# Performance work log

Hardware: AMD Instinct MI355X
Metric: run time of the kernel (lower is better)

The kernel has to match this reference:

```python
import jax, jax.numpy as jnp
import numpy as np

W_LOSS = 10.0
THRESHOLD = 1.0
ACOS_EPS = 1e-7


def _normalize(v, eps=1e-8):
    n = jnp.linalg.norm(v, axis=-1, keepdims=True)
    return v / jnp.maximum(n, eps)


def quat_to_rotmat(q):
    # q: (..., 4) in (w, x, y, z) order, as in Zhou et al. / EPN repo
    q = _normalize(q)
    w, x, y, z = q[..., 0], q[..., 1], q[..., 2], q[..., 3]
    R = jnp.stack([
        1 - 2 * (y * y + z * z), 2 * (x * y - z * w), 2 * (x * z + y * w),
        2 * (x * y + z * w), 1 - 2 * (x * x + z * z), 2 * (y * z - x * w),
        2 * (x * z - y * w), 2 * (y * z + x * w), 1 - 2 * (x * x + y * y),
    ], axis=-1)
    return R.reshape(q.shape[:-1] + (3, 3))


def acos_safe(x):
    return jnp.arccos(jnp.clip(x, -1.0 + ACOS_EPS, 1.0 - ACOS_EPS))


def angle_from_R(R):
    # R: (..., 3, 3) -> geodesic angle via trace
    tr = jnp.trace(R, axis1=-2, axis2=-1)
    return acos_safe(0.5 * (tr - 1.0))


def setup_inputs() -> dict:
    key = jax.random.key(0)
    k1, k2, k3, k4, k5 = jax.random.split(key, 5)
    B, NA, NR = 32768, 60, 4
    wts = jax.random.normal(k1, (B, NA), dtype=jnp.float32)
    label = jax.random.randint(k2, (B,), 0, NA, dtype=jnp.int64)
    y = jax.random.normal(k3, (B, NR, NA), dtype=jnp.float32)
    # gt_R and anchors are valid rotation matrices (via random quaternions)
    gt_R = quat_to_rotmat(jax.random.normal(k4, (B, NA, 4), dtype=jnp.float32))
    anchors = quat_to_rotmat(jax.random.normal(k5, (NA, 4), dtype=jnp.float32))
    return {"wts": wts, "label": label, "y": y, "gt_R": gt_R, "anchors": anchors}


def reference(wts, label, y, gt_R, anchors):
    b, na = wts.shape
    nr = y.shape[1]
    true_R = gt_R[:, 29]  # (b, 3, 3)

    # --- CrossEntropyLoss branch (classifier) ---
    logp = jax.nn.log_softmax(wts, axis=1)
    cls_loss = -jnp.mean(jnp.take_along_axis(logp, label[:, None], axis=1))
    preds = jnp.argmax(wts, axis=1)  # (b,)
    r_acc = jnp.mean((preds == label).astype(jnp.float32))

    # --- anchor-wise predicted rotations ---
    # y (b, nr, na) -> (b, na, nr) -> (b, na, 3, 3)
    pred_RAnchor = quat_to_rotmat(jnp.swapaxes(y, 1, 2))

    gt_bias = angle_from_R(gt_R)  # (b, na)
    mask = (gt_bias < THRESHOLD).astype(gt_R.dtype)[:, :, None, None]
    l2_loss = jnp.sum(jnp.square(gt_R * mask - pred_RAnchor * mask))
    loss = cls_loss + W_LOSS * l2_loss

    # --- final predicted rotation: gather best anchor, compose with anchor rot ---
    sel = jnp.take_along_axis(pred_RAnchor, preds[:, None, None, None], axis=1)[:, 0]  # (b,3,3)
    pred_R = jnp.einsum('bij,bjk->bik', anchors[preds], sel)

    # --- mean angular error ---
    ang_err = angle_from_R(jnp.einsum('bij,bkj->bik', pred_R, true_R))  # (b,)

    return (loss, cls_loss, W_LOSS * l2_loss, r_acc, ang_err)
```

## Files before the change

kernel.cpp:

```cpp
#include <hip/hip_runtime.h>
#include <math.h>

constexpr int Bc  = 32768;
constexpr int NAc = 60;
constexpr int NRc = 4;

constexpr int WPB    = 4;
constexpr int NBLK   = 2048;
constexpr int NWAVES = NBLK * WPB;

#define COS_ONE 0.5403023058681398f

__global__ __launch_bounds__(256) void mtl_main(
    const float* __restrict__ wts,
    const int*   __restrict__ label,
    const float* __restrict__ y,
    const float* __restrict__ gt_R,
    const float* __restrict__ anchors,
    float*       __restrict__ out,
    float*       __restrict__ l2p,
    float*       __restrict__ lpp,
    float*       __restrict__ crp)
{
    const int lane = threadIdx.x & 63;
    const int wave = threadIdx.x >> 6;
    const int gw   = blockIdx.x * WPB + wave;

    float l2_acc = 0.0f;
    float lp_acc = 0.0f;
    float cr_acc = 0.0f;

    for (int b = gw; b < Bc; b += NWAVES) {
        float w = -INFINITY;
        if (lane < NAc) w = wts[(size_t)b * NAc + lane];
        float mv = w;
        int   mi = lane;
        for (int off = 32; off; off >>= 1) {
            float ov = __shfl_xor(mv, off, 64);
            int   oi = __shfl_xor(mi, off, 64);
            if (ov > mv || (ov == mv && oi < mi)) { mv = ov; mi = oi; }
        }
        float e  = (lane < NAc) ? expf(w - mv) : 0.0f;
        float se = e;
        for (int off = 32; off; off >>= 1) se += __shfl_xor(se, off, 64);
        float lse  = mv + logf(se);
        int   lab  = label[b];
        float wlab = __shfl(w, lab, 64);
        if (lane == 0) {
            lp_acc += wlab - lse;
            cr_acc += (mi == lab) ? 1.0f : 0.0f;
        }

        if (lane < NAc) {
            const float* yb = y + (size_t)b * (NRc * NAc);
            float qw = yb[0 * NAc + lane];
            float qx = yb[1 * NAc + lane];
            float qy = yb[2 * NAc + lane];
            float qz = yb[3 * NAc + lane];
            float n   = sqrtf(qw * qw + qx * qx + qy * qy + qz * qz);
            float inv = 1.0f / fmaxf(n, 1e-8f);
            qw *= inv; qx *= inv; qy *= inv; qz *= inv;

            float R00 = 1.0f - 2.0f * (qy * qy + qz * qz);
            float R01 = 2.0f * (qx * qy - qz * qw);
            float R02 = 2.0f * (qx * qz + qy * qw);
            float R10 = 2.0f * (qx * qy + qz * qw);
            float R11 = 1.0f - 2.0f * (qx * qx + qz * qz);
            float R12 = 2.0f * (qy * qz - qx * qw);
            float R20 = 2.0f * (qx * qz - qy * qw);
            float R21 = 2.0f * (qy * qz + qx * qw);
            float R22 = 1.0f - 2.0f * (qx * qx + qy * qy);

            const float* g = gt_R + ((size_t)b * NAc + lane) * 9;
            float g0 = g[0], g1 = g[1], g2 = g[2];
            float g3 = g[3], g4 = g[4], g5 = g[5];
            float g6 = g[6], g7 = g[7], g8 = g[8];

            float xb = 0.5f * (g0 + g4 + g8 - 1.0f);
            if (xb > COS_ONE) {
                float d0 = g0 - R00, d1 = g1 - R01, d2 = g2 - R02;
                float d3 = g3 - R10, d4 = g4 - R11, d5 = g5 - R12;
                float d6 = g6 - R20, d7 = g7 - R21, d8 = g8 - R22;
                l2_acc += d0 * d0 + d1 * d1 + d2 * d2
                        + d3 * d3 + d4 * d4 + d5 * d5
                        + d6 * d6 + d7 * d7 + d8 * d8;
            }

            if (lane == mi) {
                const float* A = anchors + (size_t)mi * 9;
                float a0 = A[0], a1 = A[1], a2 = A[2];
                float a3 = A[3], a4 = A[4], a5 = A[5];
                float a6 = A[6], a7 = A[7], a8 = A[8];
                float P00 = a0 * R00 + a1 * R10 + a2 * R20;
                float P01 = a0 * R01 + a1 * R11 + a2 * R21;
                float P02 = a0 * R02 + a1 * R12 + a2 * R22;
                float P10 = a3 * R00 + a4 * R10 + a5 * R20;
                float P11 = a3 * R01 + a4 * R11 + a5 * R21;
                float P12 = a3 * R02 + a4 * R12 + a5 * R22;
                float P20 = a6 * R00 + a7 * R10 + a8 * R20;
                float P21 = a6 * R01 + a7 * R11 + a8 * R21;
                float P22 = a6 * R02 + a7 * R12 + a8 * R22;
                const float* tR = gt_R + ((size_t)b * NAc + 29) * 9;
                float tr = P00 * tR[0] + P01 * tR[1] + P02 * tR[2]
                         + P10 * tR[3] + P11 * tR[4] + P12 * tR[5]
                         + P20 * tR[6] + P21 * tR[7] + P22 * tR[8];
                float cx = 0.5f * (tr - 1.0f);
                cx = fminf(fmaxf(cx, -1.0f + 1e-7f), 1.0f - 1e-7f);
                out[4 + b] = acosf(cx);
            }
        }
    }

    for (int off = 32; off; off >>= 1) {
        l2_acc += __shfl_xor(l2_acc, off, 64);
        lp_acc += __shfl_xor(lp_acc, off, 64);
        cr_acc += __shfl_xor(cr_acc, off, 64);
    }
    __shared__ float s_l2[WPB], s_lp[WPB], s_cr[WPB];
    if (lane == 0) { s_l2[wave] = l2_acc; s_lp[wave] = lp_acc; s_cr[wave] = cr_acc; }
    __syncthreads();
    if (threadIdx.x == 0) {
        float t2 = 0.0f, tp = 0.0f, tc = 0.0f;
        for (int i = 0; i < WPB; ++i) { t2 += s_l2[i]; tp += s_lp[i]; tc += s_cr[i]; }
        l2p[blockIdx.x] = t2;
        lpp[blockIdx.x] = tp;
        crp[blockIdx.x] = tc;
    }
}

__global__ __launch_bounds__(64) void mtl_final(
    const float* __restrict__ l2p,
    const float* __restrict__ lpp,
    const float* __restrict__ crp,
    float*       __restrict__ out)
{
    const int lane = threadIdx.x;
    double l2 = 0.0, lp = 0.0, cr = 0.0;
    for (int i = lane; i < NBLK; i += 64) {
        l2 += (double)l2p[i];
        lp += (double)lpp[i];
        cr += (double)crp[i];
    }
    for (int off = 32; off; off >>= 1) {
        l2 += __shfl_xor(l2, off, 64);
        lp += __shfl_xor(lp, off, 64);
        cr += __shfl_xor(cr, off, 64);
    }
    if (lane == 0) {
        float cls = (float)(-lp / (double)Bc);
        float l2s = (float)(10.0 * l2);
        out[0] = cls + l2s;
        out[1] = cls;
        out[2] = l2s;
        out[3] = (float)(cr / (double)Bc);
    }
}

extern "C" void kernel_launch(void* const* d_in, const int* in_sizes, int n_in,
                              void* d_out, int out_size, void* d_ws, size_t ws_size,
                              hipStream_t stream) {
    const float* wts     = (const float*)d_in[0];
    const int*   label   = (const int*)d_in[1];
    const float* y       = (const float*)d_in[2];
    const float* gt_R    = (const float*)d_in[3];
    const float* anchors = (const float*)d_in[4];
    float* out = (float*)d_out;

    float* l2p = (float*)d_ws;
    float* lpp = l2p + NBLK;
    float* crp = lpp + NBLK;

    mtl_main<<<NBLK, 256, 0, stream>>>(wts, label, y, gt_R, anchors, out, l2p, lpp, crp);
    mtl_final<<<1, 64, 0, stream>>>(l2p, lpp, crp, out);
}
```

Baseline: 156.5 us.

## Split L2 loss into flat tiled kernel with LDS-staged coalesced gt_R loads

Splits the fused per-sample kernel in two. A flat per-(sample, anchor) L2 kernel stages 256 gt_R matrices into shared memory with float4 coalesced loads. A separate classifier and angle-error kernel computes the rotation only for the argmax lane. This removes the stride-9 uncoalesced gt_R reads and the idle lanes (60 of 64) in the heavy pass, at the cost of an extra kernel launch and re-reading y for the selected anchor.

```diff
diff --git a/kernel.cpp b/kernel.cpp
--- a/kernel.cpp
+++ b/kernel.cpp
@@ -5,32 +5,98 @@
 constexpr int NAc = 60;
 constexpr int NRc = 4;
 
-constexpr int WPB    = 4;
-constexpr int NBLK   = 2048;
-constexpr int NWAVES = NBLK * WPB;
+constexpr int NP     = Bc * NAc;
+constexpr int TILE   = 256;
+constexpr int NTILES = NP / TILE;
+constexpr int K1_BLOCKS = 3840;
+constexpr int K2_BLOCKS = 1024;
+constexpr int K2_WAVES  = K2_BLOCKS * 4;
 
 #define COS_ONE 0.5403023058681398f
 
-__global__ __launch_bounds__(256) void mtl_main(
+__global__ __launch_bounds__(256) void l2_pairs(
+    const float* __restrict__ y,
+    const float* __restrict__ gt_R,
+    float*       __restrict__ l2p)
+{
+    __shared__ float4 sg4[TILE * 9 / 4];
+    float* sg = (float*)sg4;
+    const int tid = threadIdx.x;
+
+    float acc = 0.0f;
+
+    for (int tile = blockIdx.x; tile < NTILES; tile += gridDim.x) {
+        __syncthreads();
+        const float4* gbase = (const float4*)(gt_R + (size_t)tile * (TILE * 9));
+        for (int i = tid; i < TILE * 9 / 4; i += 256) sg4[i] = gbase[i];
+        __syncthreads();
+
+        const int p = tile * TILE + tid;
+        const int b = p / NAc;
+        const int a = p - b * NAc;
+
+        const float* yb = y + (size_t)b * (NRc * NAc) + a;
+        float qw = yb[0 * NAc];
+        float qx = yb[1 * NAc];
+        float qy = yb[2 * NAc];
+        float qz = yb[3 * NAc];
+
+        const float* g = sg + tid * 9;
+        float g0 = g[0], g1 = g[1], g2 = g[2];
+        float g3 = g[3], g4 = g[4], g5 = g[5];
+        float g6 = g[6], g7 = g[7], g8 = g[8];
+
+        float n   = sqrtf(qw * qw + qx * qx + qy * qy + qz * qz);
+        float inv = 1.0f / fmaxf(n, 1e-8f);
+        qw *= inv; qx *= inv; qy *= inv; qz *= inv;
+
+        float R00 = 1.0f - 2.0f * (qy * qy + qz * qz);
+        float R01 = 2.0f * (qx * qy - qz * qw);
+        float R02 = 2.0f * (qx * qz + qy * qw);
+        float R10 = 2.0f * (qx * qy + qz * qw);
+        float R11 = 1.0f - 2.0f * (qx * qx + qz * qz);
+        float R12 = 2.0f * (qy * qz - qx * qw);
+        float R20 = 2.0f * (qx * qz - qy * qw);
+        float R21 = 2.0f * (qy * qz + qx * qw);
+        float R22 = 1.0f - 2.0f * (qx * qx + qy * qy);
+
+        float xb = 0.5f * (g0 + g4 + g8 - 1.0f);
+        if (xb > COS_ONE) {
+            float d0 = g0 - R00, d1 = g1 - R01, d2 = g2 - R02;
+            float d3 = g3 - R10, d4 = g4 - R11, d5 = g5 - R12;
+            float d6 = g6 - R20, d7 = g7 - R21, d8 = g8 - R22;
+            acc += d0 * d0 + d1 * d1 + d2 * d2
+                 + d3 * d3 + d4 * d4 + d5 * d5
+                 + d6 * d6 + d7 * d7 + d8 * d8;
+        }
+    }
+
+    for (int off = 32; off; off >>= 1) acc += __shfl_xor(acc, off, 64);
+    __shared__ float sred[4];
+    const int lane = tid & 63, wave = tid >> 6;
+    if (lane == 0) sred[wave] = acc;
+    __syncthreads();
+    if (tid == 0) l2p[blockIdx.x] = sred[0] + sred[1] + sred[2] + sred[3];
+}
+
+__global__ __launch_bounds__(256) void cls_angerr(
     const float* __restrict__ wts,
     const int*   __restrict__ label,
     const float* __restrict__ y,
     const float* __restrict__ gt_R,
     const float* __restrict__ anchors,
     float*       __restrict__ out,
-    float*       __restrict__ l2p,
     float*       __restrict__ lpp,
     float*       __restrict__ crp)
 {
     const int lane = threadIdx.x & 63;
     const int wave = threadIdx.x >> 6;
-    const int gw   = blockIdx.x * WPB + wave;
-
-    float l2_acc = 0.0f;
+    const int gw   = blockIdx.x * 4 + wave;
+
     float lp_acc = 0.0f;
     float cr_acc = 0.0f;
 
-    for (int b = gw; b < Bc; b += NWAVES) {
+    for (int b = gw; b < Bc; b += K2_WAVES) {
         float w = -INFINITY;
         if (lane < NAc) w = wts[(size_t)b * NAc + lane];
         float mv = w;
@@ -51,16 +117,15 @@
             cr_acc += (mi == lab) ? 1.0f : 0.0f;
         }
 
-        if (lane < NAc) {
-            const float* yb = y + (size_t)b * (NRc * NAc);
-            float qw = yb[0 * NAc + lane];
-            float qx = yb[1 * NAc + lane];
-            float qy = yb[2 * NAc + lane];
-            float qz = yb[3 * NAc + lane];
+        if (lane == mi) {
+            const float* yb = y + (size_t)b * (NRc * NAc) + mi;
+            float qw = yb[0 * NAc];
+            float qx = yb[1 * NAc];
+            float qy = yb[2 * NAc];
+            float qz = yb[3 * NAc];
             float n   = sqrtf(qw * qw + qx * qx + qy * qy + qz * qz);
             float inv = 1.0f / fmaxf(n, 1e-8f);
             qw *= inv; qx *= inv; qy *= inv; qz *= inv;
-
             float R00 = 1.0f - 2.0f * (qy * qy + qz * qz);
             float R01 = 2.0f * (qx * qy - qz * qw);
             float R02 = 2.0f * (qx * qz + qy * qw);
@@ -71,60 +136,39 @@
             float R21 = 2.0f * (qy * qz + qx * qw);
             float R22 = 1.0f - 2.0f * (qx * qx + qy * qy);
 
-            const float* g = gt_R + ((size_t)b * NAc + lane) * 9;
-            float g0 = g[0], g1 = g[1], g2 = g[2];
-            float g3 = g[3], g4 = g[4], g5 = g[5];
-            float g6 = g[6], g7 = g[7], g8 = g[8];
-
-            float xb = 0.5f * (g0 + g4 + g8 - 1.0f);
-            if (xb > COS_ONE) {
-                float d0 = g0 - R00, d1 = g1 - R01, d2 = g2 - R02;
-                float d3 = g3 - R10, d4 = g4 - R11, d5 = g5 - R12;
-                float d6 = g6 - R20, d7 = g7 - R21, d8 = g8 - R22;
-                l2_acc += d0 * d0 + d1 * d1 + d2 * d2
-                        + d3 * d3 + d4 * d4 + d5 * d5
-                        + d6 * d6 + d7 * d7 + d8 * d8;
-            }
-
-            if (lane == mi) {
-                const float* A = anchors + (size_t)mi * 9;
-                float a0 = A[0], a1 = A[1], a2 = A[2];
-                float a3 = A[3], a4 = A[4], a5 = A[5];
-                float a6 = A[6], a7 = A[7], a8 = A[8];
-                float P00 = a0 * R00 + a1 * R10 + a2 * R20;
-                float P01 = a0 * R01 + a1 * R11 + a2 * R21;
-                float P02 = a0 * R02 + a1 * R12 + a2 * R22;
-                float P10 = a3 * R00 + a4 * R10 + a5 * R20;
-                float P11 = a3 * R01 + a4 * R11 + a5 * R21;
-                float P12 = a3 * R02 + a4 * R12 + a5 * R22;
-                float P20 = a6 * R00 + a7 * R10 + a8 * R20;
-                float P21 = a6 * R01 + a7 * R11 + a8 * R21;
-                float P22 = a6 * R02 + a7 * R12 + a8 * R22;
-                const float* tR = gt_R + ((size_t)b * NAc + 29) * 9;
-                float tr = P00 * tR[0] + P01 * tR[1] + P02 * tR[2]
-                         + P10 * tR[3] + P11 * tR[4] + P12 * tR[5]
-                         + P20 * tR[6] + P21 * tR[7] + P22 * tR[8];
-                float cx = 0.5f * (tr - 1.0f);
-                cx = fminf(fmaxf(cx, -1.0f + 1e-7f), 1.0f - 1e-7f);
-                out[4 + b] = acosf(cx);
-            }
+            const float* A = anchors + (size_t)mi * 9;
+            float a0 = A[0], a1 = A[1], a2 = A[2];
+            float a3 = A[3], a4 = A[4], a5 = A[5];
+            float a6 = A[6], a7 = A[7], a8 = A[8];
+            float P00 = a0 * R00 + a1 * R10 + a2 * R20;
+            float P01 = a0 * R01 + a1 * R11 + a2 * R21;
+            float P02 = a0 * R02 + a1 * R12 + a2 * R22;
+            float P10 = a3 * R00 + a4 * R10 + a5 * R20;
+            float P11 = a3 * R01 + a4 * R11 + a5 * R21;
+            float P12 = a3 * R02 + a4 * R12 + a5 * R22;
+            float P20 = a6 * R00 + a7 * R10 + a8 * R20;
+            float P21 = a6 * R01 + a7 * R11 + a8 * R21;
+            float P22 = a6 * R02 + a7 * R12 + a8 * R22;
+            const float* tR = gt_R + ((size_t)b * NAc + 29) * 9;
+            float tr = P00 * tR[0] + P01 * tR[1] + P02 * tR[2]
+                     + P10 * tR[3] + P11 * tR[4] + P12 * tR[5]
+                     + P20 * tR[6] + P21 * tR[7] + P22 * tR[8];
+            float cx = 0.5f * (tr - 1.0f);
+            cx = fminf(fmaxf(cx, -1.0f + 1e-7f), 1.0f - 1e-7f);
+            out[4 + b] = acosf(cx);
         }
     }
 
     for (int off = 32; off; off >>= 1) {
-        l2_acc += __shfl_xor(l2_acc, off, 64);
         lp_acc += __shfl_xor(lp_acc, off, 64);
         cr_acc += __shfl_xor(cr_acc, off, 64);
     }
-    __shared__ float s_l2[WPB], s_lp[WPB], s_cr[WPB];
-    if (lane == 0) { s_l2[wave] = l2_acc; s_lp[wave] = lp_acc; s_cr[wave] = cr_acc; }
+    __shared__ float s_lp[4], s_cr[4];
+    if (lane == 0) { s_lp[wave] = lp_acc; s_cr[wave] = cr_acc; }
     __syncthreads();
     if (threadIdx.x == 0) {
-        float t2 = 0.0f, tp = 0.0f, tc = 0.0f;
-        for (int i = 0; i < WPB; ++i) { t2 += s_l2[i]; tp += s_lp[i]; tc += s_cr[i]; }
-        l2p[blockIdx.x] = t2;
-        lpp[blockIdx.x] = tp;
-        crp[blockIdx.x] = tc;
+        lpp[blockIdx.x] = s_lp[0] + s_lp[1] + s_lp[2] + s_lp[3];
+        crp[blockIdx.x] = s_cr[0] + s_cr[1] + s_cr[2] + s_cr[3];
     }
 }
 
@@ -136,8 +180,8 @@
 {
     const int lane = threadIdx.x;
     double l2 = 0.0, lp = 0.0, cr = 0.0;
-    for (int i = lane; i < NBLK; i += 64) {
-        l2 += (double)l2p[i];
+    for (int i = lane; i < K1_BLOCKS; i += 64) l2 += (double)l2p[i];
+    for (int i = lane; i < K2_BLOCKS; i += 64) {
         lp += (double)lpp[i];
         cr += (double)crp[i];
     }
@@ -167,9 +211,10 @@
     float* out = (float*)d_out;
 
     float* l2p = (float*)d_ws;
-    float* lpp = l2p + NBLK;
-    float* crp = lpp + NBLK;
-
-    mtl_main<<<NBLK, 256, 0, stream>>>(wts, label, y, gt_R, anchors, out, l2p, lpp, crp);
-    mtl_final<<<1, 64, 0, stream>>>(l2p, lpp, crp, out);
-}
+    float* lpp = l2p + K1_BLOCKS;
+    float* crp = lpp + K2_BLOCKS;
+
+    l2_pairs  <<<K1_BLOCKS, 256, 0, stream>>>(y, gt_R, l2p);
+    cls_angerr<<<K2_BLOCKS, 256, 0, stream>>>(wts, label, y, gt_R, anchors, out, lpp, crp);
+    mtl_final <<<1, 64, 0, stream>>>(l2p, lpp, crp, out);
+}
```

After: 172.2 us. 10.0% more time.
